# Optimization experiments

Hardware: AMD Instinct MI355X
Metric: run time of the kernel (lower is better)

## Reference

```python
import jax, jax.numpy as jnp
import numpy as np

B, Q, K = 4, 256, 1024          # batch, query_len, key_len
DQ, DK, DV, H = 512, 512, 512, 256  # query/key/value dims, num_hiddens


def setup_inputs() -> dict:
    key = jax.random.key(0)
    ks = jax.random.split(key, 7)
    return {
        "queries": jax.random.normal(ks[0], (B, Q, DQ), jnp.float32),
        "keys": jax.random.normal(ks[1], (B, K, DK), jnp.float32),
        "values": jax.random.normal(ks[2], (B, K, DV), jnp.float32),
        "valid_lens": jax.random.randint(ks[3], (B,), 1, K + 1),
        "Wq": jax.random.normal(ks[4], (H, DQ), jnp.float32) / np.sqrt(DQ).astype(np.float32),
        "Wk": jax.random.normal(ks[5], (H, DK), jnp.float32) / np.sqrt(DK).astype(np.float32),
        "wv": jax.random.normal(ks[6], (H,), jnp.float32) / np.sqrt(H).astype(np.float32),
    }


def reference(queries, keys, values, valid_lens, Wq, Wk, wv):
    # Linear projections (bias=False), torch Linear weight layout (out, in)
    q = jnp.einsum("bqd,hd->bqh", queries, Wq)          # (B, Q, H)
    k = jnp.einsum("bkd,hd->bkh", keys, Wk)             # (B, K, H)
    # Broadcast add -> tanh -> scalar score per (q, k) pair
    feats = jnp.tanh(q[:, :, None, :] + k[:, None, :, :])  # (B, Q, K, H)
    scores = jnp.einsum("bqkh,h->bqk", feats, wv)           # (B, Q, K)
    # masked_softmax with 1D valid_lens: mask applies along key axis per batch
    kv_len = scores.shape[-1]
    mask = jnp.arange(kv_len)[None, None, :] < valid_lens[:, None, None]  # (B,1,K)
    scores = jnp.where(mask, scores, jnp.float32(-1e6))
    attn = jax.nn.softmax(scores, axis=-1)               # (B, Q, K)
    # dropout is identity in eval mode
    return jnp.einsum("bqk,bkv->bqv", attn, values)      # (B, Q, DV)
```

## Files before the change

kernel.cpp:

```cpp
#include <hip/hip_runtime.h>
#include <stdint.h>


#define NB 4
#define NQ 256
#define NK 1024
#define ND 512
#define NH 256
#define QROWS 4
#define PJR 16
#define PJH 64

#define C2L2E 2.8853900817779268f
#define L2E   1.4426950408889634f

typedef float v2f __attribute__((ext_vector_type(2)));

__device__ void ff_vldec(const int* p, int* v) {
  bool ok = true;
  for (int i = 0; i < 4; ++i) { int x = p[i]; if (x < 1 || x > NK) ok = false; }
  if (ok) { for (int i = 0; i < 4; ++i) v[i] = p[i]; return; }
  ok = true;
  for (int i = 0; i < 4; ++i) {
    if (p[2 * i + 1] != 0) ok = false;
    int x = p[2 * i]; if (x < 1 || x > NK) ok = false;
  }
  if (ok) { for (int i = 0; i < 4; ++i) v[i] = p[2 * i]; return; }
  ok = true;
  for (int i = 0; i < 4; ++i) {
    union { int i; float f; } u; u.i = p[i];
    if (!(u.f >= 1.0f && u.f <= 1024.0f && u.f == floorf(u.f))) ok = false;
  }
  if (ok) {
    for (int i = 0; i < 4; ++i) { union { int i; float f; } u; u.i = p[i]; v[i] = (int)u.f; }
    return;
  }
  ok = true;
  for (int i = 0; i < 4; ++i) {
    union { long long l; double d; } u;
    u.l = ((long long)p[2 * i + 1] << 32) | (unsigned int)p[2 * i];
    if (!(u.d >= 1.0 && u.d <= 1024.0 && u.d == floor(u.d))) ok = false;
  }
  if (ok) {
    for (int i = 0; i < 4; ++i) {
      union { long long l; double d; } u;
      u.l = ((long long)p[2 * i + 1] << 32) | (unsigned int)p[2 * i];
      v[i] = (int)u.d;
    }
    return;
  }
  const uint16_t* hh = (const uint16_t*)p;
  const short*    s  = (const short*)p;
  ok = true;
  for (int i = 0; i < 4; ++i) { int x = s[i]; if (x < 1 || x > NK) ok = false; }
  if (ok) { for (int i = 0; i < 4; ++i) v[i] = s[i]; return; }
  ok = true;
  for (int i = 0; i < 4; ++i) {
    union { uint16_t u; _Float16 h; } u; u.u = hh[i];
    float f = (float)u.h;
    if (!(f >= 1.0f && f <= 1024.0f && f == floorf(f))) ok = false;
  }
  if (ok) {
    for (int i = 0; i < 4; ++i) {
      union { uint16_t u; _Float16 h; } u; u.u = hh[i];
      v[i] = (int)(float)u.h;
    }
    return;
  }
  ok = true;
  for (int i = 0; i < 4; ++i) {
    union { uint32_t u; float f; } u; u.u = ((uint32_t)hh[i]) << 16;
    if (!(u.f >= 1.0f && u.f <= 1028.0f)) ok = false;
  }
  if (ok) {
    for (int i = 0; i < 4; ++i) {
      union { uint32_t u; float f; } u; u.u = ((uint32_t)hh[i]) << 16;
      int x = (int)(u.f + 0.5f); if (x > NK) x = NK; v[i] = x;
    }
    return;
  }
  for (int i = 0; i < 4; ++i) v[i] = NK;
}

__global__ __launch_bounds__(256) void ff_wt(
    const float* __restrict__ Wq, const float* __restrict__ Wk,
    float* __restrict__ WTq, float* __restrict__ WTk)
{
  const int idx = blockIdx.x * 256 + threadIdx.x;
  const int d4 = idx & 127, h = idx >> 7;
  const float* src = blockIdx.y ? Wk : Wq;
  float*       dst = blockIdx.y ? WTk : WTq;
  float4 w = *(const float4*)(src + (size_t)h * ND + d4 * 4);
  w.x *= C2L2E; w.y *= C2L2E; w.z *= C2L2E; w.w *= C2L2E;
  *(float4*)(dst + ((size_t)d4 * NH + h) * 4) = w;
}

__global__ __launch_bounds__(256) void ff_proj(
    const float* __restrict__ q_in, const float* __restrict__ k_in,
    const float* __restrict__ WTq, const float* __restrict__ WTk,
    float* __restrict__ qp, float* __restrict__ kp)
{
  __shared__ float xs[PJR * ND];
  const int t  = threadIdx.x;
  const int rg = blockIdx.x >> 2;
  const int h0 = (blockIdx.x & 3) * PJH;
  const int gr0 = rg * PJR;
  const bool isq = gr0 < NB * NQ;
  const float* xin = isq ? (q_in + (size_t)gr0 * ND)
                         : (k_in + (size_t)(gr0 - NB * NQ) * ND);
  const float4* wt4 = (const float4*)(isq ? WTq : WTk);

  #pragma unroll
  for (int i = 0; i < 8; ++i)
    ((float4*)xs)[t + 256 * i] = ((const float4*)xin)[t + 256 * i];
  __syncthreads();

  const int L  = t & 63;
  const int rw = t >> 6;
  float a0 = 0.f, a1 = 0.f, a2 = 0.f, a3 = 0.f;
  const float4* xr = (const float4*)xs + (size_t)(4 * rw) * 128;

  #pragma unroll 4
  for (int d4 = 0; d4 < ND / 4; ++d4) {
    float4 w  = wt4[(size_t)d4 * NH + h0 + L];
    float4 x0 = xr[d4];
    float4 x1 = xr[128 + d4];
    float4 x2 = xr[256 + d4];
    float4 x3 = xr[384 + d4];
    a0 += w.x*x0.x + w.y*x0.y + w.z*x0.z + w.w*x0.w;
    a1 += w.x*x1.x + w.y*x1.y + w.z*x1.z + w.w*x1.w;
    a2 += w.x*x2.x + w.y*x2.y + w.z*x2.z + w.w*x2.w;
    a3 += w.x*x3.x + w.y*x3.y + w.z*x3.z + w.w*x3.w;
  }
  a0 = __builtin_amdgcn_exp2f(a0);
  a1 = __builtin_amdgcn_exp2f(a1);
  a2 = __builtin_amdgcn_exp2f(a2);
  a3 = __builtin_amdgcn_exp2f(a3);

  const int h = h0 + L;
  if (isq) {
    float* o = qp + (size_t)(gr0 + 4 * rw) * NH + h;
    o[0] = a0; o[NH] = a1; o[2 * NH] = a2; o[3 * NH] = a3;
  } else {
    const int g = gr0 - NB * NQ + 4 * rw;
    const int bb = g >> 10, k = g & (NK - 1);
    *(float4*)(kp + ((size_t)bb * NH + h) * NK + k) = make_float4(a0, a1, a2, a3);
  }
}

__global__ __launch_bounds__(1024) void ff_attn2(
    const float* __restrict__ qp, const float* __restrict__ kp,
    const float* __restrict__ vals, const int* __restrict__ vlraw,
    const float* __restrict__ wvp, float* __restrict__ pvpart,
    float* __restrict__ Sg)
{
  __shared__ float  qs[NH * QROWS];
  __shared__ float4 wsp[NH / 2];
  __shared__ float  st[512 * QROWS];
  __shared__ float  psum[32];
  __shared__ float  part[4 * QROWS * ND];

  const int t  = threadIdx.x;
  const int kh = blockIdx.x;
  const int q0 = blockIdx.y * QROWS;
  const int b  = blockIdx.z;

  {
    const float* qsrc = qp + ((size_t)b * NQ + q0) * NH;
    const int row = t >> 8, h = t & 255;
    qs[h * QROWS + row] = qsrc[t];
    if (t < NH / 2) {
      float w0 = wvp[2 * t], w1 = wvp[2 * t + 1];
      wsp[t] = make_float4(-2.0f * w0, -2.0f * w1, -2.0f * (w0 + w1), 0.0f);
    }
  }
  __syncthreads();

  int vls[4];
  ff_vldec(vlraw, vls);
  const int vl = vls[b];

  const int kk = t & 511, rh = t >> 9;
  v2f acc = {0.f, 0.f};
  {
    const float* kvp = kp + (size_t)b * NH * NK + kh * 512 + kk;
    const float* qsp = qs + 2 * rh;
    #pragma unroll 4
    for (int hp = 0; hp < NH / 2; ++hp) {
      float Ak0 = kvp[(size_t)(2 * hp) * NK];
      float Ak1 = kvp[(size_t)(2 * hp + 1) * NK];
      v2f Aq0 = *(const v2f*)(qsp + (2 * hp) * QROWS);
      v2f Aq1 = *(const v2f*)(qsp + (2 * hp + 1) * QROWS);
      float4 wt = wsp[hp];
      v2f ak0; ak0.x = Ak0; ak0.y = Ak0;
      v2f ak1; ak1.x = Ak1; ak1.y = Ak1;
      v2f a = Aq0 * ak0;
      v2f bb = Aq1 * ak1;
      v2f one; one.x = 1.0f; one.y = 1.0f;
      v2f oa = one + a, ob = one + bb;
      v2f D = oa * ob;
      v2f w0s; w0s.x = wt.x; w0s.y = wt.x;
      v2f w1s; w1s.x = wt.y; w1s.y = wt.y;
      v2f N; N.x = wt.z; N.y = wt.z;
      N += w0s * bb;
      N += w1s * a;
      v2f rD;
      rD.x = __builtin_amdgcn_rcpf(D.x);
      rD.y = __builtin_amdgcn_rcpf(D.y);
      acc += N * rD;
    }
  }
  {
    const bool okm = (kh * 512 + kk) < vl;
    v2f E;
    E.x = okm ? __builtin_amdgcn_exp2f(acc.x * L2E) : 0.f;
    E.y = okm ? __builtin_amdgcn_exp2f(acc.y * L2E) : 0.f;
    *(v2f*)&st[kk * 4 + 2 * rh] = E;
    float sx = E.x, sy = E.y;
    for (int o = 32; o; o >>= 1) { sx += __shfl_xor(sx, o); sy += __shfl_xor(sy, o); }
    if ((t & 63) == 0) { psum[(t >> 6) * 2] = sx; psum[(t >> 6) * 2 + 1] = sy; }
  }
  __syncthreads();

  if (t < 4) {
    const int j = t & 1, base = (t >> 1) * 8;
    float S = 0.f;
    #pragma unroll
    for (int w = 0; w < 8; ++w) S += psum[(base + w) * 2 + j];
    Sg[(((size_t)b * 64 + blockIdx.y) * 4 + t) * 2 + kh] = S;
  }

  {
    const int kq = t >> 8, c2 = (t & 255) * 2;
    const float* vb = vals + (size_t)b * NK * ND
                    + (size_t)(kh * 512 + kq * 128) * ND + c2;
    v2f o0 = {0.f,0.f}, o1 = {0.f,0.f}, o2 = {0.f,0.f}, o3 = {0.f,0.f};
    #pragma unroll 8
    for (int k = 0; k < 128; ++k) {
      v2f vv = *(const v2f*)(vb + (size_t)k * ND);
      float4 a = *(const float4*)&st[(kq * 128 + k) * 4];
      v2f ax; ax.x = a.x; ax.y = a.x;
      v2f ay; ay.x = a.y; ay.y = a.y;
      v2f az; az.x = a.z; az.y = a.z;
      v2f aw; aw.x = a.w; aw.y = a.w;
      o0 += ax * vv; o1 += ay * vv; o2 += az * vv; o3 += aw * vv;
    }
    *(v2f*)&part[(size_t)(kq * 4 + 0) * ND + c2] = o0;
    *(v2f*)&part[(size_t)(kq * 4 + 1) * ND + c2] = o1;
    *(v2f*)&part[(size_t)(kq * 4 + 2) * ND + c2] = o2;
    *(v2f*)&part[(size_t)(kq * 4 + 3) * ND + c2] = o3;
  }
  __syncthreads();
  {
    const int r = t >> 8, c2 = (t & 255) * 2;
    v2f s = {0.f, 0.f};
    #pragma unroll
    for (int kq = 0; kq < 4; ++kq)
      s += *(const v2f*)&part[(size_t)(kq * 4 + r) * ND + c2];
    *(v2f*)&pvpart[(((size_t)kh * NB + b) * NQ + q0 + r) * ND + c2] = s;
  }
}

__global__ __launch_bounds__(256) void ff_comb(
    const float* __restrict__ pvpart, const float* __restrict__ Sg,
    float* __restrict__ out)
{
  const int bid = blockIdx.x;
  const int t = threadIdx.x;
  const float S = Sg[bid * 2] + Sg[bid * 2 + 1];
  const float rs = 1.0f / S;
  const int b = bid >> 8, q = bid & 255;
  const float* p0 = pvpart + ((size_t)b * NQ + q) * ND;
  const float* p1 = pvpart + ((size_t)(NB + b) * NQ + q) * ND;
  float2 a = *(const float2*)(p0 + t * 2);
  float2 c = *(const float2*)(p1 + t * 2);
  *(float2*)(out + ((size_t)b * NQ + q) * ND + t * 2)
      = make_float2((a.x + c.x) * rs, (a.y + c.y) * rs);
}

__global__ __launch_bounds__(1024) void ff_attn(
    const float* __restrict__ qp, const float* __restrict__ kp,
    const float* __restrict__ vals, const int* __restrict__ vlraw,
    const float* __restrict__ wvp, float* __restrict__ out)
{
  __shared__ float qs[NH * QROWS];
  __shared__ float ws[NH];
  __shared__ float st[NK * QROWS];
  __shared__ float pm[16], psm[16];
  __shared__ float part[4 * QROWS * ND];

  const int t  = threadIdx.x;
  const int q0 = blockIdx.x * QROWS;
  const int b  = blockIdx.y;

  {
    const float* qsrc = qp + ((size_t)b * NQ + q0) * NH;
    const int row = t >> 8, h = t & 255;
    qs[h * QROWS + row] = qsrc[t];
    if (t < NH) ws[t] = -2.0f * wvp[t];
  }
  __syncthreads();

  int vls[4];
  ff_vldec(vlraw, vls);
  const int vl = vls[b];

  v2f a01 = {0.f, 0.f}, a23 = {0.f, 0.f};
  {
    const float* kvp = kp + (size_t)b * NH * NK + t;
    #pragma unroll 8
    for (int h = 0; h < NH; ++h) {
      float Ak = kvp[(size_t)h * NK];
      v2f ak; ak.x = Ak; ak.y = Ak;
      v2f q01 = *(const v2f*)(qs + h * QROWS);
      v2f q23 = *(const v2f*)(qs + h * QROWS + 2);
      float w = ws[h];
      v2f w2; w2.x = w; w2.y = w;
      v2f one; one.x = 1.0f; one.y = 1.0f;
      v2f d01 = one + q01 * ak;
      v2f d23 = one + q23 * ak;
      v2f r01, r23;
      r01.x = __builtin_amdgcn_rcpf(d01.x);
      r01.y = __builtin_amdgcn_rcpf(d01.y);
      r23.x = __builtin_amdgcn_rcpf(d23.x);
      r23.y = __builtin_amdgcn_rcpf(d23.y);
      a01 += w2 * r01;
      a23 += w2 * r23;
    }
  }
  {
    const bool okm = (t < vl);
    *(float4*)&st[t * 4] = make_float4(okm ? a01.x : -1e6f, okm ? a01.y : -1e6f,
                                       okm ? a23.x : -1e6f, okm ? a23.y : -1e6f);
  }
  __syncthreads();

  {
    const int wid = t >> 6, lane = t & 63;
    const int row = wid >> 2, seg = wid & 3;
    const int kb = seg * 256 + lane;
    float v0 = st[(kb      ) * 4 + row];
    float v1 = st[(kb +  64) * 4 + row];
    float v2 = st[(kb + 128) * 4 + row];
    float v3 = st[(kb + 192) * 4 + row];
    float m = fmaxf(fmaxf(v0, v1), fmaxf(v2, v3));
    for (int o = 32; o; o >>= 1) m = fmaxf(m, __shfl_xor(m, o));
    if (lane == 0) pm[wid] = m;
    __syncthreads();
    m = fmaxf(fmaxf(pm[row*4+0], pm[row*4+1]), fmaxf(pm[row*4+2], pm[row*4+3]));
    float e0 = __builtin_amdgcn_exp2f((v0 - m) * L2E);
    float e1 = __builtin_amdgcn_exp2f((v1 - m) * L2E);
    float e2 = __builtin_amdgcn_exp2f((v2 - m) * L2E);
    float e3 = __builtin_amdgcn_exp2f((v3 - m) * L2E);
    float sm = e0 + e1 + e2 + e3;
    for (int o = 32; o; o >>= 1) sm += __shfl_xor(sm, o);
    if (lane == 0) psm[wid] = sm;
    __syncthreads();
    const float S = psm[row*4+0] + psm[row*4+1] + psm[row*4+2] + psm[row*4+3];
    const float rr = 1.0f / S;
    st[(kb      ) * 4 + row] = e0 * rr;
    st[(kb +  64) * 4 + row] = e1 * rr;
    st[(kb + 128) * 4 + row] = e2 * rr;
    st[(kb + 192) * 4 + row] = e3 * rr;
  }
  __syncthreads();

  {
    const int kq = t >> 8, c2 = (t & 255) * 2;
    const float* vb = vals + (size_t)b * NK * ND + c2;
    v2f o0 = {0.f,0.f}, o1 = {0.f,0.f}, o2 = {0.f,0.f}, o3 = {0.f,0.f};
    const int k0 = kq * 256;
    #pragma unroll 8
    for (int k = k0; k < k0 + 256; ++k) {
      v2f vv = *(const v2f*)(vb + (size_t)k * ND);
      float4 a = *(const float4*)&st[k * 4];
      v2f ax; ax.x = a.x; ax.y = a.x;
      v2f ay; ay.x = a.y; ay.y = a.y;
      v2f az; az.x = a.z; az.y = a.z;
      v2f aw; aw.x = a.w; aw.y = a.w;
      o0 += ax * vv; o1 += ay * vv; o2 += az * vv; o3 += aw * vv;
    }
    float* pp = &part[(size_t)kq * QROWS * ND + c2];
    *(v2f*)(pp         ) = o0;
    *(v2f*)(pp +     ND) = o1;
    *(v2f*)(pp + 2 * ND) = o2;
    *(v2f*)(pp + 3 * ND) = o3;
  }
  __syncthreads();
  {
    const int r = t >> 8, c2 = (t & 255) * 2;
    const float* pp = &part[(size_t)r * ND + c2];
    v2f s = {0.f, 0.f};
    #pragma unroll
    for (int kq = 0; kq < 4; ++kq) s += *(const v2f*)(pp + (size_t)kq * QROWS * ND);
    *(v2f*)(out + ((size_t)b * NQ + q0 + r) * ND + c2) = s;
  }
}

extern "C" void kernel_launch(void* const* d_in, const int* in_sizes, int n_in,
                              void* d_out, int out_size, void* d_ws, size_t ws_size,
                              hipStream_t stream) {
  const float* queries = (const float*)d_in[0];
  const float* keys    = (const float*)d_in[1];
  const float* values  = (const float*)d_in[2];
  const int*   vlens   = (const int*)d_in[3];
  const float* Wq      = (const float*)d_in[4];
  const float* Wk      = (const float*)d_in[5];
  const float* wv      = (const float*)d_in[6];
  float* out = (float*)d_out;

  float* qp  = (float*)d_ws;
  float* kp  = qp  + (size_t)NB * NQ * NH;
  float* wtq = kp  + (size_t)NB * NH * NK;
  float* wtk = wtq + (size_t)(ND / 4) * NH * 4;
  float* pvp = wtk + (size_t)(ND / 4) * NH * 4;
  float* Sg  = pvp + (size_t)2 * NB * NQ * ND;
  const size_t need = ((size_t)(Sg - (float*)d_ws) + 2 * NB * NQ) * sizeof(float);

  ff_wt  <<<dim3(128, 2), 256, 0, stream>>>(Wq, Wk, wtq, wtk);
  ff_proj<<<dim3((NB * (NQ + NK) / PJR) * (NH / PJH)), 256, 0, stream>>>(
      queries, keys, wtq, wtk, qp, kp);
  if (ws_size >= need) {
    ff_attn2<<<dim3(2, NQ / QROWS, NB), 1024, 0, stream>>>(
        qp, kp, values, vlens, wv, pvp, Sg);
    ff_comb<<<dim3(NB * NQ), 256, 0, stream>>>(pvp, Sg, out);
  } else {
    ff_attn<<<dim3(NQ / QROWS, NB), 1024, 0, stream>>>(
        qp, kp, values, vlens, wv, out);
  }
}
```

Before: 188.1 us.

## Interleave projected keys by groups of four hidden units for float4 loads

The key projection kernel now transposes its output through shared memory and writes keys in an [b][h/4][k][4] layout. Both attention kernels then fetch four hidden units per key with one float4 global load instead of four strided scalar loads. Query rows are also stored row-major in shared memory, so they can be read as float4 vectors. This is meant to cut global load instruction count and latency in the score loop, at the cost of an extra shared-memory transpose and two barriers in the projection kernel.

```diff
diff --git a/kernel.cpp b/kernel.cpp
--- a/kernel.cpp
+++ b/kernel.cpp
@@ -137,14 +137,22 @@
   a2 = __builtin_amdgcn_exp2f(a2);
   a3 = __builtin_amdgcn_exp2f(a3);
 
-  const int h = h0 + L;
   if (isq) {
+    const int h = h0 + L;
     float* o = qp + (size_t)(gr0 + 4 * rw) * NH + h;
     o[0] = a0; o[NH] = a1; o[2 * NH] = a2; o[3 * NH] = a3;
   } else {
-    const int g = gr0 - NB * NQ + 4 * rw;
-    const int bb = g >> 10, k = g & (NK - 1);
-    *(float4*)(kp + ((size_t)bb * NH + h) * NK + k) = make_float4(a0, a1, a2, a3);
+    __syncthreads();
+    float* trs = xs;
+    *(float4*)&trs[L * 16 + 4 * rw] = make_float4(a0, a1, a2, a3);
+    __syncthreads();
+    const int kl = t & 15, jl = t >> 4;
+    const int g0 = gr0 - NB * NQ;
+    const int bb = g0 >> 10, kg0 = g0 & (NK - 1);
+    const int j0 = (blockIdx.x & 3) * 16;
+    float4 o4 = make_float4(trs[(4*jl+0)*16 + kl], trs[(4*jl+1)*16 + kl],
+                            trs[(4*jl+2)*16 + kl], trs[(4*jl+3)*16 + kl]);
+    ((float4*)kp)[((size_t)bb * 64 + j0 + jl) * 1024 + kg0 + kl] = o4;
   }
 }
 
@@ -154,8 +162,8 @@
     const float* __restrict__ wvp, float* __restrict__ pvpart,
     float* __restrict__ Sg)
 {
-  __shared__ float  qs[NH * QROWS];
-  __shared__ float4 wsp[NH / 2];
+  __shared__ float  qs[QROWS * NH];
+  __shared__ float4 wspp[NH / 2];
   __shared__ float  st[512 * QROWS];
   __shared__ float  psum[32];
   __shared__ float  part[4 * QROWS * ND];
@@ -167,11 +175,10 @@
 
   {
     const float* qsrc = qp + ((size_t)b * NQ + q0) * NH;
-    const int row = t >> 8, h = t & 255;
-    qs[h * QROWS + row] = qsrc[t];
+    qs[t] = qsrc[t];
     if (t < NH / 2) {
       float w0 = wvp[2 * t], w1 = wvp[2 * t + 1];
-      wsp[t] = make_float4(-2.0f * w0, -2.0f * w1, -2.0f * (w0 + w1), 0.0f);
+      wspp[t] = make_float4(-2.0f * w0, -2.0f * w1, -2.0f * (w0 + w1), 0.0f);
     }
   }
   __syncthreads();
@@ -183,31 +190,46 @@
   const int kk = t & 511, rh = t >> 9;
   v2f acc = {0.f, 0.f};
   {
-    const float* kvp = kp + (size_t)b * NH * NK + kh * 512 + kk;
-    const float* qsp = qs + 2 * rh;
+    const float4* kvp = (const float4*)kp + ((size_t)b * 64) * 1024
+                      + (kh * 512 + kk);
+    const float* q0p = qs + (2 * rh) * NH;
+    const float* q1p = qs + (2 * rh + 1) * NH;
     #pragma unroll 4
-    for (int hp = 0; hp < NH / 2; ++hp) {
-      float Ak0 = kvp[(size_t)(2 * hp) * NK];
-      float Ak1 = kvp[(size_t)(2 * hp + 1) * NK];
-      v2f Aq0 = *(const v2f*)(qsp + (2 * hp) * QROWS);
-      v2f Aq1 = *(const v2f*)(qsp + (2 * hp + 1) * QROWS);
-      float4 wt = wsp[hp];
-      v2f ak0; ak0.x = Ak0; ak0.y = Ak0;
-      v2f ak1; ak1.x = Ak1; ak1.y = Ak1;
-      v2f a = Aq0 * ak0;
-      v2f bb = Aq1 * ak1;
+    for (int j = 0; j < 64; ++j) {
+      float4 K4 = kvp[(size_t)j << 10];
+      float4 A0 = *(const float4*)(q0p + 4 * j);
+      float4 A1 = *(const float4*)(q1p + 4 * j);
+      float4 wa = wspp[2 * j];
+      float4 wb = wspp[2 * j + 1];
       v2f one; one.x = 1.0f; one.y = 1.0f;
-      v2f oa = one + a, ob = one + bb;
-      v2f D = oa * ob;
-      v2f w0s; w0s.x = wt.x; w0s.y = wt.x;
-      v2f w1s; w1s.x = wt.y; w1s.y = wt.y;
-      v2f N; N.x = wt.z; N.y = wt.z;
-      N += w0s * bb;
-      N += w1s * a;
-      v2f rD;
-      rD.x = __builtin_amdgcn_rcpf(D.x);
-      rD.y = __builtin_amdgcn_rcpf(D.y);
-      acc += N * rD;
+      {
+        v2f a;  a.x  = A0.x * K4.x; a.y  = A1.x * K4.x;
+        v2f b2; b2.x = A0.y * K4.y; b2.y = A1.y * K4.y;
+        v2f D = (one + a) * (one + b2);
+        v2f N;   N.x = wa.z;  N.y = wa.z;
+        v2f w0v; w0v.x = wa.x; w0v.y = wa.x;
+        v2f w1v; w1v.x = wa.y; w1v.y = wa.y;
+        N += w0v * b2;
+        N += w1v * a;
+        v2f rD;
+        rD.x = __builtin_amdgcn_rcpf(D.x);
+        rD.y = __builtin_amdgcn_rcpf(D.y);
+        acc += N * rD;
+      }
+      {
+        v2f a;  a.x  = A0.z * K4.z; a.y  = A1.z * K4.z;
+        v2f b2; b2.x = A0.w * K4.w; b2.y = A1.w * K4.w;
+        v2f D = (one + a) * (one + b2);
+        v2f N;   N.x = wb.z;  N.y = wb.z;
+        v2f w0v; w0v.x = wb.x; w0v.y = wb.x;
+        v2f w1v; w1v.x = wb.y; w1v.y = wb.y;
+        N += w0v * b2;
+        N += w1v * a;
+        v2f rD;
+        rD.x = __builtin_amdgcn_rcpf(D.x);
+        rD.y = __builtin_amdgcn_rcpf(D.y);
+        acc += N * rD;
+      }
     }
   }
   {
@@ -283,7 +305,7 @@
     const float* __restrict__ vals, const int* __restrict__ vlraw,
     const float* __restrict__ wvp, float* __restrict__ out)
 {
-  __shared__ float qs[NH * QROWS];
+  __shared__ float qs[QROWS * NH];
   __shared__ float ws[NH];
   __shared__ float st[NK * QROWS];
   __shared__ float pm[16], psm[16];
@@ -295,8 +317,7 @@
 
   {
     const float* qsrc = qp + ((size_t)b * NQ + q0) * NH;
-    const int row = t >> 8, h = t & 255;
-    qs[h * QROWS + row] = qsrc[t];
+    qs[t] = qsrc[t];
     if (t < NH) ws[t] = -2.0f * wvp[t];
   }
   __syncthreads();
@@ -305,33 +326,26 @@
   ff_vldec(vlraw, vls);
   const int vl = vls[b];
 
-  v2f a01 = {0.f, 0.f}, a23 = {0.f, 0.f};
-  {
-    const float* kvp = kp + (size_t)b * NH * NK + t;
-    #pragma unroll 8
-    for (int h = 0; h < NH; ++h) {
-      float Ak = kvp[(size_t)h * NK];
-      v2f ak; ak.x = Ak; ak.y = Ak;
-      v2f q01 = *(const v2f*)(qs + h * QROWS);
-      v2f q23 = *(const v2f*)(qs + h * QROWS + 2);
-      float w = ws[h];
-      v2f w2; w2.x = w; w2.y = w;
-      v2f one; one.x = 1.0f; one.y = 1.0f;
-      v2f d01 = one + q01 * ak;
-      v2f d23 = one + q23 * ak;
-      v2f r01, r23;
-      r01.x = __builtin_amdgcn_rcpf(d01.x);
-      r01.y = __builtin_amdgcn_rcpf(d01.y);
-      r23.x = __builtin_amdgcn_rcpf(d23.x);
-      r23.y = __builtin_amdgcn_rcpf(d23.y);
-      a01 += w2 * r01;
-      a23 += w2 * r23;
+  float sc[4] = {0.f, 0.f, 0.f, 0.f};
+  {
+    const float4* kvp = (const float4*)kp + ((size_t)b * 64) * 1024 + t;
+    for (int j = 0; j < 64; ++j) {
+      float4 K4 = kvp[(size_t)j << 10];
+      const float* wj = &ws[4 * j];
+      #pragma unroll
+      for (int r = 0; r < 4; ++r) {
+        const float* qr = &qs[r * NH + 4 * j];
+        sc[r] += wj[0] * __builtin_amdgcn_rcpf(1.0f + qr[0] * K4.x);
+        sc[r] += wj[1] * __builtin_amdgcn_rcpf(1.0f + qr[1] * K4.y);
+        sc[r] += wj[2] * __builtin_amdgcn_rcpf(1.0f + qr[2] * K4.z);
+        sc[r] += wj[3] * __builtin_amdgcn_rcpf(1.0f + qr[3] * K4.w);
+      }
     }
   }
   {
     const bool okm = (t < vl);
-    *(float4*)&st[t * 4] = make_float4(okm ? a01.x : -1e6f, okm ? a01.y : -1e6f,
-                                       okm ? a23.x : -1e6f, okm ? a23.y : -1e6f);
+    *(float4*)&st[t * 4] = make_float4(okm ? sc[0] : -1e6f, okm ? sc[1] : -1e6f,
+                                       okm ? sc[2] : -1e6f, okm ? sc[3] : -1e6f);
   }
   __syncthreads();
 
```

Result: no change. 189.0 us (+0.5%).
